# Kernel optimization log

Hardware: AMD Instinct MI355X
Metric: run time of the kernel (lower is better)

The kernel has to match this reference:

```python
import jax, jax.numpy as jnp
import numpy as np

N = 50000      # nodes
E = 600000     # edges
IN = 128       # in_channels
HID = 128      # GCN hidden width (fixed in module)
H = 4          # TransformerConv heads
C = 32         # out_channels per head (heads*C = 128)


def _lin(k, fan_in, fan_out):
    return jax.random.normal(k, (fan_in, fan_out), jnp.float32) / np.sqrt(fan_in)


def setup_inputs() -> dict:
    key = jax.random.key(0)
    ks = jax.random.split(key, 12)
    return {
        "x": jax.random.normal(ks[0], (N, IN), jnp.float32),
        "edge_index": jax.random.randint(ks[1], (2, E), 0, N, dtype=jnp.int32),
        "W_gcn": _lin(ks[2], IN, HID),
        "b_gcn": jnp.zeros((HID,), jnp.float32),
        "Wq": _lin(ks[3], HID, H * C),
        "bq": jnp.zeros((H * C,), jnp.float32),
        "Wk": _lin(ks[4], HID, H * C),
        "bk": jnp.zeros((H * C,), jnp.float32),
        "Wv": _lin(ks[5], HID, H * C),
        "bv": jnp.zeros((H * C,), jnp.float32),
        "Ws": _lin(ks[6], HID, H * C),
        "bs": jnp.zeros((H * C,), jnp.float32),
    }


def reference(x, edge_index, W_gcn, b_gcn, Wq, bq, Wk, bk, Wv, bv, Ws, bs):
    n = x.shape[0]
    idt = edge_index.dtype

    # ---- GCNConv: x' = D^{-1/2}(A+I)D^{-1/2} x W + b, then ReLU ----
    h = x @ W_gcn                                   # [N, HID] linear first (PyG order)
    loop = jnp.arange(n, dtype=idt)
    src = jnp.concatenate([edge_index[0], loop])    # with self-loops
    tgt = jnp.concatenate([edge_index[1], loop])
    deg = jax.ops.segment_sum(jnp.ones(src.shape, h.dtype), tgt, num_segments=n)
    dinv = jnp.where(deg > 0, jax.lax.rsqrt(deg), 0.0)
    norm = dinv[src] * dinv[tgt]                    # [E+N]
    h = jax.ops.segment_sum(h[src] * norm[:, None], tgt, num_segments=n)
    h = jax.nn.relu(h + b_gcn)                      # [N, HID]

    # ---- TransformerConv (heads=4, concat=True, no self-loops added) ----
    s, t = edge_index[0], edge_index[1]
    q = (h @ Wq + bq).reshape(n, H, C)
    k = (h @ Wk + bk).reshape(n, H, C)
    v = (h @ Wv + bv).reshape(n, H, C)

    alpha = jnp.einsum('ehc,ehc->eh', q[t], k[s]) / np.sqrt(C)   # [E, H]
    m = jax.lax.stop_gradient(jax.ops.segment_max(alpha, t, num_segments=n))
    ea = jnp.exp(alpha - m[t])
    denom = jax.ops.segment_sum(ea, t, num_segments=n)           # [N, H]
    w = ea / jnp.where(denom[t] > 0, denom[t], 1.0)              # softmax per target node

    out = jax.ops.segment_sum(w[:, :, None] * v[s], t, num_segments=n)  # [N, H, C]
    out = out.reshape(n, H * C)

    # root/skip connection (lin_skip)
    return out + h @ Ws + bs
```

## Files before the change

kernel.cpp:

```cpp
#include <hip/hip_runtime.h>
#include <hip/hip_bf16.h>

typedef __attribute__((ext_vector_type(8))) short short8;
typedef __attribute__((ext_vector_type(4))) float floatx4;
typedef _Float16 half2v __attribute__((ext_vector_type(2)));

__device__ __forceinline__ float ld_f(const void* p, int f32, int i) {
  if (f32) return ((const float*)p)[i];
  unsigned short u = ((const unsigned short*)p)[i];
  return __uint_as_float(((unsigned)u) << 16);
}
__device__ __forceinline__ short ld_bf(const void* p, int f32, int i) {
  if (!f32) return ((const short*)p)[i];
  __hip_bfloat16 h = __float2bfloat16(((const float*)p)[i]);
  return *reinterpret_cast<short*>(&h);
}
__device__ __forceinline__ unsigned short f_to_bfu(float v) {
  __hip_bfloat16 h = __float2bfloat16(v);
  return *reinterpret_cast<unsigned short*>(&h);
}
__device__ __forceinline__ short f_to_h(float v) {
  _Float16 h = (_Float16)v;
  return *reinterpret_cast<short*>(&h);
}
__device__ __forceinline__ float bflo(unsigned w) { return __uint_as_float(w << 16); }
__device__ __forceinline__ float bfhi(unsigned w) { return __uint_as_float(w & 0xFFFF0000u); }

__global__ void init_kernel(const unsigned short* __restrict__ xs, int* __restrict__ flag,
                            int* __restrict__ cnt, int N) {
  if (blockIdx.x == 0) {
    __shared__ int sbad;
    if (threadIdx.x == 0) sbad = 0;
    __syncthreads();
    int bad = 0;
    for (int j = 2 * threadIdx.x; j < 16384; j += 512) {
      unsigned e = (xs[j] >> 7) & 0xFF;
      if (e >= 0xF0) bad = 1;
    }
    if (bad) atomicOr(&sbad, 1);
    __syncthreads();
    if (threadIdx.x == 0) flag[0] = sbad;
    return;
  }
  int i = (blockIdx.x - 1) * blockDim.x + threadIdx.x;
  if (i < N) cnt[i] = 0;
}

__global__ void prep_hist(const void* bg, const void* bq, const void* bk, const void* bv,
                          const void* bs, const void* Wg, const void* Wq, const void* Wk,
                          const void* Wv, const void* Ws, const int* __restrict__ flag,
                          float* __restrict__ bgf, float* __restrict__ bias512,
                          short* __restrict__ WpG, short* __restrict__ WpQ,
                          const int* __restrict__ ei, int* __restrict__ cnt,
                          int* __restrict__ erank, int E, int Gp) {
  if ((int)blockIdx.x >= Gp) {
    int e = (blockIdx.x - Gp) * blockDim.x + threadIdx.x;
    if (e < E) erank[e] = atomicAdd(&cnt[ei[E + e]], 1);
    return;
  }
  int tid = blockIdx.x * blockDim.x + threadIdx.x;
  int f = *flag;
  if (tid < 128) { bgf[tid] = ld_f(bg, f, tid); return; }
  if (tid < 640) {
    int t = tid - 128;
    const void* b = (t < 128) ? bq : (t < 256) ? bk : (t < 384) ? bv : bs;
    bias512[t] = ld_f(b, f, t & 127);
    return;
  }
  if (tid < 640 + 2048) {
    int id = tid - 640;
    int lane = id & 63, kb = (id >> 6) & 3, tn = id >> 8;
    int k0 = kb * 32 + (lane >> 4) * 8;
    int n = tn * 16 + (lane & 15);
    short* dst = WpG + (size_t)id * 8;
#pragma unroll
    for (int j = 0; j < 8; ++j) dst[j] = ld_bf(Wg, f, (k0 + j) * 128 + n);
    return;
  }
  if (tid < 640 + 2048 + 8192) {
    int id = tid - 640 - 2048;
    int lane = id & 63, kb = (id >> 6) & 3, tn = id >> 8;
    int k0 = kb * 32 + (lane >> 4) * 8;
    int n = tn * 16 + (lane & 15);
    const void* W = (n < 128) ? Wq : (n < 256) ? Wk : (n < 384) ? Wv : Ws;
    int col = n & 127;
    short* dst = WpQ + (size_t)id * 8;
#pragma unroll
    for (int j = 0; j < 8; ++j) dst[j] = ld_bf(W, f, (k0 + j) * 128 + col);
  }
}

__global__ void scanA(const int* __restrict__ cnt, int* __restrict__ chunkscan,
                      int* __restrict__ partials, int N) {
  __shared__ int sh[1024];
  int t = threadIdx.x;
  int g = blockIdx.x * 1024 + t;
  int v = (g < N) ? cnt[g] : 0;
  sh[t] = v;
  __syncthreads();
  for (int o = 1; o < 1024; o <<= 1) {
    int add = (t >= o) ? sh[t - o] : 0;
    __syncthreads();
    sh[t] += add;
    __syncthreads();
  }
  if (g < N) chunkscan[g] = sh[t];
  if (t == 1023) partials[blockIdx.x] = sh[1023];
}

__global__ void scanB(int* __restrict__ partials, int nb) {
  int lane = threadIdx.x;
  if (nb <= 64) {
    int v = (lane < nb) ? partials[lane] : 0;
#pragma unroll
    for (int o = 1; o < 64; o <<= 1) {
      int t = __shfl_up(v, o);
      if (lane >= o) v += t;
    }
    int ex = __shfl_up(v, 1);
    if (lane == 0) ex = 0;
    if (lane < nb) partials[lane] = ex;
    return;
  }
  if (lane == 0) {
    int run = 0;
    for (int b = 0; b < nb; ++b) {
      int t = partials[b];
      partials[b] = run;
      run += t;
    }
  }
}

__global__ void scanC(const int* __restrict__ cnt, const int* __restrict__ chunkscan,
                      const int* __restrict__ partials, int* __restrict__ rowptr,
                      float* __restrict__ dinv, int N) {
  int g = blockIdx.x * blockDim.x + threadIdx.x;
  if (g == 0) rowptr[0] = 0;
  if (g >= N) return;
  int c = cnt[g];
  int inc = chunkscan[g] + partials[g >> 10];
  rowptr[g + 1] = inc;
  dinv[g] = rsqrtf((float)c + 1.0f);
}

__global__ void gemmh0_fill(const void* __restrict__ X, const int* __restrict__ flag,
                            const short* __restrict__ Bp, const float* __restrict__ dinv,
                            short* __restrict__ C, int M, const int* __restrict__ ei,
                            const int* __restrict__ rowptr, const int* __restrict__ erank,
                            int* __restrict__ srcs, int E, int Gg) {
  if ((int)blockIdx.x >= Gg) {
    int e = (blockIdx.x - Gg) * blockDim.x + threadIdx.x;
    if (e < E) {
      int t = ei[E + e];
      srcs[rowptr[t] + erank[e]] = ei[e];
    }
    return;
  }
  int wv = (blockIdx.x * blockDim.x + threadIdx.x) >> 6;
  int lane = threadIdx.x & 63;
  int tilesM = (M + 15) >> 4;
  if (wv >= tilesM) return;
  int f = *flag;
  int tm = wv;
  int m = tm * 16 + (lane & 15);
  int mc = m < M ? m : M - 1;
  int quad = lane >> 4;
  short8 a[4];
  if (f) {
    const float4* xr = (const float4*)((const float*)X + (size_t)mc * 128) + quad * 2;
#pragma unroll
    for (int kb = 0; kb < 4; ++kb) {
      float4 u = xr[kb * 8];
      float4 w = xr[kb * 8 + 1];
      a[kb][0] = (short)f_to_bfu(u.x);
      a[kb][1] = (short)f_to_bfu(u.y);
      a[kb][2] = (short)f_to_bfu(u.z);
      a[kb][3] = (short)f_to_bfu(u.w);
      a[kb][4] = (short)f_to_bfu(w.x);
      a[kb][5] = (short)f_to_bfu(w.y);
      a[kb][6] = (short)f_to_bfu(w.z);
      a[kb][7] = (short)f_to_bfu(w.w);
    }
  } else {
    const short* xr = (const short*)X + (size_t)mc * 128 + quad * 8;
#pragma unroll
    for (int kb = 0; kb < 4; ++kb) a[kb] = *(const short8*)(xr + kb * 32);
  }
  floatx4 acc[8];
#pragma unroll
  for (int tn = 0; tn < 8; ++tn) acc[tn] = (floatx4){0.f, 0.f, 0.f, 0.f};
#pragma unroll
  for (int kb = 0; kb < 4; ++kb) {
#pragma unroll
    for (int tn = 0; tn < 8; ++tn) {
      short8 b8 = *(const short8*)(Bp + ((size_t)(tn * 4 + kb) * 64 + lane) * 8);
      acc[tn] = __builtin_amdgcn_mfma_f32_16x16x32_bf16(a[kb], b8, acc[tn], 0, 0, 0);
    }
  }
  int row0 = tm * 16 + quad * 4;
  int cl = lane & 15;
  float dsc[4];
#pragma unroll
  for (int r = 0; r < 4; ++r) dsc[r] = (row0 + r < M) ? dinv[row0 + r] : 0.f;
#pragma unroll
  for (int tn = 0; tn < 8; ++tn)
#pragma unroll
    for (int r = 0; r < 4; ++r)
      if (row0 + r < M)
        C[(size_t)(row0 + r) * 128 + tn * 16 + cl] = (short)f_to_bfu(acc[tn][r] * dsc[r]);
}

__global__ void gcn_gather(const int* __restrict__ rowptr, const int* __restrict__ srcs,
                           const float* __restrict__ dinv, const unsigned* __restrict__ h0,
                           const float* __restrict__ bgf, unsigned* __restrict__ hbf, int N) {
  int wv = (int)((blockIdx.x * (long long)blockDim.x + threadIdx.x) >> 6);
  int lane = threadIdx.x & 63;
  int hf = lane >> 5, q2 = (lane >> 4) & 1, sl = lane & 15, sl32 = lane & 31;
  int node = wv * 2 + hf;
  int nodec = node < N ? node : N - 1;
  int beg = rowptr[nodec], end = rowptr[nodec + 1];
  int deg = node < N ? end - beg : 0;
  int dm1 = deg - 1;
  int dmc = dm1 > 0 ? dm1 : 0;
  int sreg = srcs[deg > 0 ? beg + (sl32 < dm1 ? sl32 : dm1) : 0];
  int degmax = deg;
  degmax = max(degmax, __shfl_xor(degmax, 32));
  int dd = degmax < 32 ? degmax : 32;
  int hb = hf << 5;
  float a0 = 0.f, a1 = 0.f, a2 = 0.f, a3 = 0.f, a4 = 0.f, a5 = 0.f, a6 = 0.f, a7 = 0.f;
  for (int base = 0; base < dd; base += 8) {
    int p0 = base + q2, p1 = p0 + 2, p2 = p0 + 4, p3 = p0 + 6;
    int s0 = __shfl(sreg, hb + (p0 < dmc ? p0 : dmc));
    int s1 = __shfl(sreg, hb + (p1 < dmc ? p1 : dmc));
    int s2 = __shfl(sreg, hb + (p2 < dmc ? p2 : dmc));
    int s3 = __shfl(sreg, hb + (p3 < dmc ? p3 : dmc));
    float m0 = p0 < deg ? 1.f : 0.f;
    float m1 = p1 < deg ? 1.f : 0.f;
    float m2 = p2 < deg ? 1.f : 0.f;
    float m3 = p3 < deg ? 1.f : 0.f;
    uint4 w0 = *(const uint4*)(h0 + (size_t)s0 * 64 + sl * 4);
    uint4 w1 = *(const uint4*)(h0 + (size_t)s1 * 64 + sl * 4);
    uint4 w2 = *(const uint4*)(h0 + (size_t)s2 * 64 + sl * 4);
    uint4 w3 = *(const uint4*)(h0 + (size_t)s3 * 64 + sl * 4);
    a0 += m0 * bflo(w0.x) + m1 * bflo(w1.x) + m2 * bflo(w2.x) + m3 * bflo(w3.x);
    a1 += m0 * bfhi(w0.x) + m1 * bfhi(w1.x) + m2 * bfhi(w2.x) + m3 * bfhi(w3.x);
    a2 += m0 * bflo(w0.y) + m1 * bflo(w1.y) + m2 * bflo(w2.y) + m3 * bflo(w3.y);
    a3 += m0 * bfhi(w0.y) + m1 * bfhi(w1.y) + m2 * bfhi(w2.y) + m3 * bfhi(w3.y);
    a4 += m0 * bflo(w0.z) + m1 * bflo(w1.z) + m2 * bflo(w2.z) + m3 * bflo(w3.z);
    a5 += m0 * bfhi(w0.z) + m1 * bfhi(w1.z) + m2 * bfhi(w2.z) + m3 * bfhi(w3.z);
    a6 += m0 * bflo(w0.w) + m1 * bflo(w1.w) + m2 * bflo(w2.w) + m3 * bflo(w3.w);
    a7 += m0 * bfhi(w0.w) + m1 * bfhi(w1.w) + m2 * bfhi(w2.w) + m3 * bfhi(w3.w);
  }
  for (int i = beg + 32 + q2; i < end; i += 2) {
    uint4 w0 = *(const uint4*)(h0 + (size_t)srcs[i] * 64 + sl * 4);
    a0 += bflo(w0.x);
    a1 += bfhi(w0.x);
    a2 += bflo(w0.y);
    a3 += bfhi(w0.y);
    a4 += bflo(w0.z);
    a5 += bfhi(w0.z);
    a6 += bflo(w0.w);
    a7 += bfhi(w0.w);
  }
  a0 += __shfl_xor(a0, 16);
  a1 += __shfl_xor(a1, 16);
  a2 += __shfl_xor(a2, 16);
  a3 += __shfl_xor(a3, 16);
  a4 += __shfl_xor(a4, 16);
  a5 += __shfl_xor(a5, 16);
  a6 += __shfl_xor(a6, 16);
  a7 += __shfl_xor(a7, 16);
  if (q2 == 0 && node < N) {
    uint4 hw = *(const uint4*)(h0 + (size_t)node * 64 + sl * 4);
    float dt = dinv[node];
    const float4* bb = (const float4*)bgf;
    float4 b0 = bb[sl * 2], b1 = bb[sl * 2 + 1];
    float v0 = (a0 + bflo(hw.x)) * dt + b0.x;
    float v1 = (a1 + bfhi(hw.x)) * dt + b0.y;
    float v2 = (a2 + bflo(hw.y)) * dt + b0.z;
    float v3 = (a3 + bfhi(hw.y)) * dt + b0.w;
    float v4 = (a4 + bflo(hw.z)) * dt + b1.x;
    float v5 = (a5 + bfhi(hw.z)) * dt + b1.y;
    float v6 = (a6 + bflo(hw.w)) * dt + b1.z;
    float v7 = (a7 + bfhi(hw.w)) * dt + b1.w;
    v0 = v0 > 0.f ? v0 : 0.f;
    v1 = v1 > 0.f ? v1 : 0.f;
    v2 = v2 > 0.f ? v2 : 0.f;
    v3 = v3 > 0.f ? v3 : 0.f;
    v4 = v4 > 0.f ? v4 : 0.f;
    v5 = v5 > 0.f ? v5 : 0.f;
    v6 = v6 > 0.f ? v6 : 0.f;
    v7 = v7 > 0.f ? v7 : 0.f;
    uint4 o;
    o.x = (unsigned)f_to_bfu(v0) | ((unsigned)f_to_bfu(v1) << 16);
    o.y = (unsigned)f_to_bfu(v2) | ((unsigned)f_to_bfu(v3) << 16);
    o.z = (unsigned)f_to_bfu(v4) | ((unsigned)f_to_bfu(v5) << 16);
    o.w = (unsigned)f_to_bfu(v6) | ((unsigned)f_to_bfu(v7) << 16);
    *(uint4*)(hbf + (size_t)node * 64 + sl * 4) = o;
  }
}

__global__ void gemm_qkvs(const short* __restrict__ A, const short* __restrict__ Bp,
                          const float* __restrict__ bias512, short* __restrict__ qb,
                          short* __restrict__ kvb, short* __restrict__ skipb, int M) {
  int wv = (blockIdx.x * blockDim.x + threadIdx.x) >> 6;
  int lane = threadIdx.x & 63;
  int tilesM = (M + 15) >> 4;
  if (wv >= tilesM * 4) return;
  int tng = wv & 3, tm = wv >> 2;
  int m = tm * 16 + (lane & 15);
  int mc = m < M ? m : M - 1;
  int quad = lane >> 4;
  const short* Arow = A + (size_t)mc * 128 + quad * 8;
  short8 a[4];
#pragma unroll
  for (int kb = 0; kb < 4; ++kb) a[kb] = *(const short8*)(Arow + kb * 32);
  floatx4 acc[8];
#pragma unroll
  for (int j = 0; j < 8; ++j) acc[j] = (floatx4){0.f, 0.f, 0.f, 0.f};
#pragma unroll
  for (int kb = 0; kb < 4; ++kb) {
#pragma unroll
    for (int j = 0; j < 8; ++j) {
      int tn = tng * 8 + j;
      short8 b8 = *(const short8*)(Bp + ((size_t)(tn * 4 + kb) * 64 + lane) * 8);
      acc[j] = __builtin_amdgcn_mfma_f32_16x16x32_bf16(a[kb], b8, acc[j], 0, 0, 0);
    }
  }
  int row0 = tm * 16 + quad * 4;
  int cl = lane & 15;
#pragma unroll
  for (int j = 0; j < 8; ++j) {
    int cc = j * 16 + cl;
    float b = bias512[tng * 128 + cc];
#pragma unroll
    for (int r = 0; r < 4; ++r) {
      int row = row0 + r;
      if (row >= M) continue;
      float val = acc[j][r] + b;
      if (tng == 0) {
        qb[(size_t)row * 128 + cc] = f_to_h(val);
      } else if (tng == 3) {
        skipb[(size_t)row * 128 + cc] = (short)f_to_bfu(val);
      } else {
        size_t base = (size_t)row * 256 + (size_t)((cc >> 2) * 8 + (cc & 3));
        if (tng == 1)
          kvb[base] = f_to_h(val);
        else
          kvb[base + 4] = (short)f_to_bfu(val);
      }
    }
  }
}

__device__ __forceinline__ float dpp_red8(float p) {
  p += __int_as_float(__builtin_amdgcn_mov_dpp(__float_as_int(p), 0xB1, 0xF, 0xF, true));
  p += __int_as_float(__builtin_amdgcn_mov_dpp(__float_as_int(p), 0x4E, 0xF, 0xF, true));
  p += __int_as_float(__builtin_amdgcn_mov_dpp(__float_as_int(p), 0x141, 0xF, 0xF, true));
  return p;
}
__device__ __forceinline__ float dot_dpp(half2v qa, half2v qc, unsigned kw0, unsigned kw1) {
  half2v k0 = *reinterpret_cast<half2v*>(&kw0);
  half2v k1 = *reinterpret_cast<half2v*>(&kw1);
#if __has_builtin(__builtin_amdgcn_fdot2)
  float p = __builtin_amdgcn_fdot2(qa, k0, 0.f, false);
  p = __builtin_amdgcn_fdot2(qc, k1, p, false);
#else
  float p = (float)qa[0] * (float)k0[0] + (float)qa[1] * (float)k0[1] +
            (float)qc[0] * (float)k1[0] + (float)qc[1] * (float)k1[1];
#endif
  return dpp_red8(p) * 0.17677669529663687f;
}

__global__ void attn_fused(const int* __restrict__ rowptr, const int* __restrict__ srcs,
                           const unsigned* __restrict__ qb, const unsigned* __restrict__ kvb,
                           const unsigned* __restrict__ skipb, float* __restrict__ out, int N) {
  int node = (int)((blockIdx.x * (long long)blockDim.x + threadIdx.x) >> 6);
  if (node >= N) return;
  int lane = threadIdx.x & 63;
  int hf = lane >> 5, sl = lane & 31;
  uint2 qw = *(const uint2*)(qb + (size_t)node * 64 + sl * 2);
  half2v qa = *reinterpret_cast<half2v*>(&qw.x);
  half2v qc = *reinterpret_cast<half2v*>(&qw.y);
  int beg = rowptr[node], end = rowptr[node + 1];
  int deg = end - beg;
  int dm1 = deg - 1;
  int dmc = dm1 > 0 ? dm1 : 0;
  int sreg = srcs[deg > 0 ? beg + (lane < dm1 ? lane : dm1) : 0];
  int dd = deg < 64 ? deg : 64;

  float denom = 0.f, ax0 = 0.f, ax1 = 0.f, ax2 = 0.f, ax3 = 0.f;
  for (int base = 0; base < dd; base += 16) {
    uint4 kv[8];
    int pp[8];
#pragma unroll
    for (int j = 0; j < 8; ++j) {
      int p = base + hf + 2 * j;
      pp[j] = p;
      int s = __shfl(sreg, p < dmc ? p : dmc);
      kv[j] = *(const uint4*)(kvb + (size_t)s * 128 + sl * 4);
    }
#pragma unroll
    for (int j = 0; j < 8; ++j) {
      float e = __expf(dot_dpp(qa, qc, kv[j].x, kv[j].y));
      e = pp[j] < deg ? e : 0.f;
      denom += e;
      ax0 += e * bflo(kv[j].z);
      ax1 += e * bfhi(kv[j].z);
      ax2 += e * bflo(kv[j].w);
      ax3 += e * bfhi(kv[j].w);
    }
  }
  for (int i = beg + 64 + hf; i < end; i += 2) {
    int s0 = srcs[i];
    uint4 kv0 = *(const uint4*)(kvb + (size_t)s0 * 128 + sl * 4);
    float e0 = __expf(dot_dpp(qa, qc, kv0.x, kv0.y));
    denom += e0;
    ax0 += e0 * bflo(kv0.z);
    ax1 += e0 * bfhi(kv0.z);
    ax2 += e0 * bflo(kv0.w);
    ax3 += e0 * bfhi(kv0.w);
  }
  denom += __shfl_xor(denom, 32);
  ax0 += __shfl_xor(ax0, 32);
  ax1 += __shfl_xor(ax1, 32);
  ax2 += __shfl_xor(ax2, 32);
  ax3 += __shfl_xor(ax3, 32);
  if (hf == 0) {
    float r = denom > 0.f ? 1.f / denom : 0.f;
    uint2 sw = *(const uint2*)(skipb + (size_t)node * 64 + sl * 2);
    float4 o;
    o.x = ax0 * r + bflo(sw.x);
    o.y = ax1 * r + bfhi(sw.x);
    o.z = ax2 * r + bflo(sw.y);
    o.w = ax3 * r + bfhi(sw.y);
    *(float4*)(out + (size_t)node * 128 + sl * 4) = o;
  }
}

extern "C" void kernel_launch(void* const* d_in, const int* in_sizes, int n_in,
                              void* d_out, int out_size, void* d_ws, size_t ws_size,
                              hipStream_t stream) {
  const void* x  = d_in[0];
  const int* ei  = (const int*)d_in[1];
  const void* Wg = d_in[2];
  const void* bg = d_in[3];
  const void* Wq = d_in[4];
  const void* bq = d_in[5];
  const void* Wk = d_in[6];
  const void* bk = d_in[7];
  const void* Wv = d_in[8];
  const void* bv = d_in[9];
  const void* Ws = d_in[10];
  const void* bs = d_in[11];
  float* out = (float*)d_out;

  const int N = in_sizes[0] / 128;
  const int E = in_sizes[1] / 2;
  int tilesM = (N + 15) / 16;
  int nscan = (N + 1023) / 1024;
  const int B = 256;

  char* ws = (char*)d_ws;
  size_t off = 0;
  auto carve = [&](size_t bytes) -> void* {
    void* p = ws + off;
    off += (bytes + 255) & ~(size_t)255;
    return p;
  };
  int* flag = (int*)carve(256);
  float* bias512 = (float*)carve(512 * 4);
  float* bgf = (float*)carve(128 * 4);
  float* dinv = (float*)carve((size_t)N * 4);
  int* cnt = (int*)carve((size_t)N * 4);
  int* rowptr = (int*)carve((size_t)(N + 1) * 4);
  int* chunkscan = (int*)carve((size_t)N * 4);
  int* partials = (int*)carve((size_t)(nscan + 1) * 4);
  int* srcs = (int*)carve((size_t)E * 4);
  int* erank = (int*)carve((size_t)E * 4);
  short* WpG = (short*)carve((size_t)16384 * 2);
  short* WpQ = (short*)carve((size_t)65536 * 2);
  short* h0bf = (short*)carve((size_t)N * 128 * 2);
  short* hbf = (short*)carve((size_t)N * 128 * 2);
  short* qb = (short*)carve((size_t)N * 128 * 2);
  short* kvb = (short*)carve((size_t)N * 256 * 2);
  short* skipb = (short*)carve((size_t)N * 128 * 2);

  int Gp = (10880 + B - 1) / B;
  int Gh = (E + B - 1) / B;
  int Gg = (tilesM * 64 + B - 1) / B;
  int Gf = (E + B - 1) / B;

  init_kernel<<<1 + (N + B - 1) / B, B, 0, stream>>>((const unsigned short*)x, flag, cnt, N);
  prep_hist<<<Gp + Gh, B, 0, stream>>>(bg, bq, bk, bv, bs, Wg, Wq, Wk, Wv, Ws, flag,
                                       bgf, bias512, WpG, WpQ, ei, cnt, erank, E, Gp);
  scanA<<<nscan, 1024, 0, stream>>>(cnt, chunkscan, partials, N);
  scanB<<<1, 64, 0, stream>>>(partials, nscan);
  scanC<<<(N + B - 1) / B, B, 0, stream>>>(cnt, chunkscan, partials, rowptr, dinv, N);
  gemmh0_fill<<<Gg + Gf, B, 0, stream>>>(x, flag, WpG, dinv, h0bf, N, ei, rowptr, erank,
                                         srcs, E, Gg);
  gcn_gather<<<(N + 7) / 8, B, 0, stream>>>(rowptr, srcs, dinv, (const unsigned*)h0bf, bgf,
                                            (unsigned*)hbf, N);
  gemm_qkvs<<<(tilesM * 4 + 3) / 4, B, 0, stream>>>(hbf, WpQ, bias512, qb, kvb, skipb, N);
  attn_fused<<<(N + 3) / 4, B, 0, stream>>>(rowptr, srcs, (const unsigned*)qb,
                                            (const unsigned*)kvb, (const unsigned*)skipb, out, N);
}
```

Baseline: 263.7 us.

## Fuse GCN neighbor gather with QKV/skip projection GEMM via shared memory tile

Merges the GCN aggregation kernel and the QKV+skip projection GEMM into one kernel. Each 512-thread block gathers 16 node rows into LDS, then its 8 waves each compute a quarter of one of the four 128-column outputs with MFMA. This removes the global write and re-read of the intermediate bf16 hidden tensor and one kernel launch. In exchange it adds a block barrier and makes blocks larger, which may lower occupancy or let the irregular gather stall the GEMM phase.

```diff
diff --git a/kernel.cpp b/kernel.cpp
--- a/kernel.cpp
+++ b/kernel.cpp
@@ -211,13 +211,18 @@
         C[(size_t)(row0 + r) * 128 + tn * 16 + cl] = (short)f_to_bfu(acc[tn][r] * dsc[r]);
 }
 
-__global__ void gcn_gather(const int* __restrict__ rowptr, const int* __restrict__ srcs,
-                           const float* __restrict__ dinv, const unsigned* __restrict__ h0,
-                           const float* __restrict__ bgf, unsigned* __restrict__ hbf, int N) {
-  int wv = (int)((blockIdx.x * (long long)blockDim.x + threadIdx.x) >> 6);
+__global__ __launch_bounds__(512) void gather_qkvs(
+    const int* __restrict__ rowptr, const int* __restrict__ srcs,
+    const float* __restrict__ dinv, const unsigned* __restrict__ h0,
+    const float* __restrict__ bgf, const short* __restrict__ Bp,
+    const float* __restrict__ bias512, short* __restrict__ qb,
+    short* __restrict__ kvb, short* __restrict__ skipb, int N) {
+  __shared__ short hsm[16][136];
+  int tileBase = blockIdx.x * 16;
+  int wv = threadIdx.x >> 6;
   int lane = threadIdx.x & 63;
   int hf = lane >> 5, q2 = (lane >> 4) & 1, sl = lane & 15, sl32 = lane & 31;
-  int node = wv * 2 + hf;
+  int node = tileBase + wv * 2 + hf;
   int nodec = node < N ? node : N - 1;
   int beg = rowptr[nodec], end = rowptr[nodec + 1];
   int deg = node < N ? end - beg : 0;
@@ -271,9 +276,9 @@
   a5 += __shfl_xor(a5, 16);
   a6 += __shfl_xor(a6, 16);
   a7 += __shfl_xor(a7, 16);
-  if (q2 == 0 && node < N) {
-    uint4 hw = *(const uint4*)(h0 + (size_t)node * 64 + sl * 4);
-    float dt = dinv[node];
+  if (q2 == 0) {
+    uint4 hw = *(const uint4*)(h0 + (size_t)nodec * 64 + sl * 4);
+    float dt = dinv[nodec];
     const float4* bb = (const float4*)bgf;
     float4 b0 = bb[sl * 2], b1 = bb[sl * 2 + 1];
     float v0 = (a0 + bflo(hw.x)) * dt + b0.x;
@@ -297,47 +302,38 @@
     o.y = (unsigned)f_to_bfu(v2) | ((unsigned)f_to_bfu(v3) << 16);
     o.z = (unsigned)f_to_bfu(v4) | ((unsigned)f_to_bfu(v5) << 16);
     o.w = (unsigned)f_to_bfu(v6) | ((unsigned)f_to_bfu(v7) << 16);
-    *(uint4*)(hbf + (size_t)node * 64 + sl * 4) = o;
-  }
-}
-
-__global__ void gemm_qkvs(const short* __restrict__ A, const short* __restrict__ Bp,
-                          const float* __restrict__ bias512, short* __restrict__ qb,
-                          short* __restrict__ kvb, short* __restrict__ skipb, int M) {
-  int wv = (blockIdx.x * blockDim.x + threadIdx.x) >> 6;
-  int lane = threadIdx.x & 63;
-  int tilesM = (M + 15) >> 4;
-  if (wv >= tilesM * 4) return;
-  int tng = wv & 3, tm = wv >> 2;
-  int m = tm * 16 + (lane & 15);
-  int mc = m < M ? m : M - 1;
+    *(uint4*)(&hsm[wv * 2 + hf][sl * 8]) = o;
+  }
+  __syncthreads();
+  int mrow = lane & 15;
   int quad = lane >> 4;
-  const short* Arow = A + (size_t)mc * 128 + quad * 8;
   short8 a[4];
 #pragma unroll
-  for (int kb = 0; kb < 4; ++kb) a[kb] = *(const short8*)(Arow + kb * 32);
-  floatx4 acc[8];
-#pragma unroll
-  for (int j = 0; j < 8; ++j) acc[j] = (floatx4){0.f, 0.f, 0.f, 0.f};
+  for (int kb = 0; kb < 4; ++kb)
+    a[kb] = *(const short8*)(&hsm[mrow][quad * 8 + kb * 32]);
+  floatx4 acc[4];
+#pragma unroll
+  for (int j = 0; j < 4; ++j) acc[j] = (floatx4){0.f, 0.f, 0.f, 0.f};
 #pragma unroll
   for (int kb = 0; kb < 4; ++kb) {
 #pragma unroll
-    for (int j = 0; j < 8; ++j) {
-      int tn = tng * 8 + j;
+    for (int j = 0; j < 4; ++j) {
+      int tn = wv * 4 + j;
       short8 b8 = *(const short8*)(Bp + ((size_t)(tn * 4 + kb) * 64 + lane) * 8);
       acc[j] = __builtin_amdgcn_mfma_f32_16x16x32_bf16(a[kb], b8, acc[j], 0, 0, 0);
     }
   }
-  int row0 = tm * 16 + quad * 4;
+  int row0 = tileBase + quad * 4;
   int cl = lane & 15;
-#pragma unroll
-  for (int j = 0; j < 8; ++j) {
-    int cc = j * 16 + cl;
+  int tng = wv >> 1;
+#pragma unroll
+  for (int j = 0; j < 4; ++j) {
+    int cc = ((wv & 1) * 4 + j) * 16 + cl;
     float b = bias512[tng * 128 + cc];
 #pragma unroll
     for (int r = 0; r < 4; ++r) {
       int row = row0 + r;
-      if (row >= M) continue;
+      if (row >= N) continue;
       float val = acc[j][r] + b;
       if (tng == 0) {
         qb[(size_t)row * 128 + cc] = f_to_h(val);
@@ -482,7 +478,6 @@
   short* WpG = (short*)carve((size_t)16384 * 2);
   short* WpQ = (short*)carve((size_t)65536 * 2);
   short* h0bf = (short*)carve((size_t)N * 128 * 2);
-  short* hbf = (short*)carve((size_t)N * 128 * 2);
   short* qb = (short*)carve((size_t)N * 128 * 2);
   short* kvb = (short*)carve((size_t)N * 256 * 2);
   short* skipb = (short*)carve((size_t)N * 128 * 2);
@@ -500,9 +495,8 @@
   scanC<<<(N + B - 1) / B, B, 0, stream>>>(cnt, chunkscan, partials, rowptr, dinv, N);
   gemmh0_fill<<<Gg + Gf, B, 0, stream>>>(x, flag, WpG, dinv, h0bf, N, ei, rowptr, erank,
                                          srcs, E, Gg);
-  gcn_gather<<<(N + 7) / 8, B, 0, stream>>>(rowptr, srcs, dinv, (const unsigned*)h0bf, bgf,
-                                            (unsigned*)hbf, N);
-  gemm_qkvs<<<(tilesM * 4 + 3) / 4, B, 0, stream>>>(hbf, WpQ, bias512, qb, kvb, skipb, N);
+  gather_qkvs<<<tilesM, 512, 0, stream>>>(rowptr, srcs, dinv, (const unsigned*)h0bf, bgf,
+                                          WpQ, bias512, qb, kvb, skipb, N);
   attn_fused<<<(N + 3) / 4, B, 0, stream>>>(rowptr, srcs, (const unsigned*)qb,
                                             (const unsigned*)kvb, (const unsigned*)skipb, out, N);
 }
```

Result: faster. 246.3 us (-6.6%).
